# Optimization experiments

Hardware: AMD Instinct MI355X
Metric: run time of the kernel (lower is better)

Reference implementation:

```python
import jax, jax.numpy as jnp
import numpy as np

N_HEAD = 16


def setup_inputs() -> dict:
    key = jax.random.key(0)
    ks = jax.random.split(key, 12)
    B, T, S, D = 64, 1, 448, 1024
    x = jax.random.normal(ks[0], (B, T, D), dtype=jnp.float32)
    k_cache = jax.random.normal(ks[1], (B, S, D), dtype=jnp.float32)
    v_cache = jax.random.normal(ks[2], (B, S, D), dtype=jnp.float32)
    current_index = jax.random.randint(ks[3], (1,), 0, S, dtype=jnp.int64)
    attention_mask = jnp.zeros((1, S), dtype=jnp.float32)
    s = 0.02
    Wq = jax.random.normal(ks[4], (D, D), dtype=jnp.float32) * s
    bq = jax.random.normal(ks[5], (D,), dtype=jnp.float32) * s
    Wk = jax.random.normal(ks[6], (D, D), dtype=jnp.float32) * s  # whisper key proj has no bias
    Wv = jax.random.normal(ks[7], (D, D), dtype=jnp.float32) * s
    bv = jax.random.normal(ks[8], (D,), dtype=jnp.float32) * s
    Wo = jax.random.normal(ks[9], (D, D), dtype=jnp.float32) * s
    bo = jax.random.normal(ks[10], (D,), dtype=jnp.float32) * s
    return {"x": x, "k_cache": k_cache, "v_cache": v_cache,
            "current_index": current_index, "attention_mask": attention_mask,
            "Wq": Wq, "bq": bq, "Wk": Wk, "Wv": Wv, "bv": bv, "Wo": Wo, "bo": bo}


def reference(x, k_cache, v_cache, current_index, attention_mask,
              Wq, bq, Wk, Wv, bv, Wo, bo):
    B, T, D = x.shape            # T == 1 (single decode token)
    S = k_cache.shape[1]         # cache length (448)
    H = N_HEAD
    Dh = D // H
    scale = float(Dh) ** -0.25

    # q/k/v projections of the new token
    q = x @ Wq + bq              # [B, T, D]
    k = x @ Wk                   # [B, T, D]
    v = x @ Wv + bv              # [B, T, D]

    # scatter the new token into the caches at current_index (functional clone+write)
    idx = current_index[0]
    k_upd = jax.lax.dynamic_update_slice(k_cache, k, (0, idx, 0))  # [B, S, D]
    v_upd = jax.lax.dynamic_update_slice(v_cache, v, (0, idx, 0))

    # whisper qkv_attention: scale q and k each by Dh**-0.25
    qh = q.reshape(B, T, H, Dh).transpose(0, 2, 1, 3) * scale      # [B, H, T, Dh]
    kh = k_upd.reshape(B, S, H, Dh).transpose(0, 2, 3, 1) * scale  # [B, H, Dh, S]
    vh = v_upd.reshape(B, S, H, Dh).transpose(0, 2, 1, 3)          # [B, H, S, Dh]

    qk = qh @ kh + attention_mask          # [B, H, T, S]  (mask broadcasts)
    w = jax.nn.softmax(qk, axis=-1)
    wv = (w @ vh).transpose(0, 2, 1, 3).reshape(B, T, D)

    out = wv @ Wo + bo
    return out, k_upd, v_upd
```

## Files before the change

### kernel.cpp

```cpp
#include <hip/hip_runtime.h>

#define B_SZ    64
#define S_LEN   448
#define D_MODEL 1024
#define N_HEAD  16
#define D_HEAD  64
#define CHUNK   28
#define NCH     16

typedef float f4 __attribute__((ext_vector_type(4)));

__global__ __launch_bounds__(256) void gemm_part(
    const float* __restrict__ X,
    const float* __restrict__ W0, const float* __restrict__ W1,
    const float* __restrict__ W2,
    float* __restrict__ P)
{
    const int nt  = blockIdx.x;
    const int kt  = blockIdx.y;
    const int mat = blockIdx.z;
    const float* __restrict__ W = (mat == 0) ? W0 : ((mat == 1) ? W1 : W2);

    const int t  = threadIdx.x;
    const int n  = nt * 64 + (t & 63);
    const int b0 = __builtin_amdgcn_readfirstlane((t >> 6) * 16);
    const int k0 = kt * 128;

    float acc[16];
#pragma unroll
    for (int j = 0; j < 16; ++j) acc[j] = 0.f;

#pragma unroll 8
    for (int k = k0; k < k0 + 128; ++k) {
        const float w = W[k * D_MODEL + n];
#pragma unroll
        for (int j = 0; j < 16; ++j)
            acc[j] += X[(b0 + j) * D_MODEL + k] * w;
    }

    float* p = P + (size_t)(mat * 8 + kt) * (B_SZ * D_MODEL);
#pragma unroll
    for (int j = 0; j < 16; ++j)
        p[(b0 + j) * D_MODEL + n] = acc[j];
}

__global__ __launch_bounds__(256) void reduce_qkv(
    const float* __restrict__ P, float* __restrict__ out)
{
    const int i   = blockIdx.x * 256 + threadIdx.x;
    const int mat = i >> 16;
    const int r   = i & 65535;
    float s = 0.f;
#pragma unroll
    for (int kt = 0; kt < 8; ++kt)
        s += P[(size_t)(mat * 8 + kt) * 65536 + r];
    out[i] = s;
}

__global__ __launch_bounds__(256) void reduce_out(
    const float* __restrict__ P, const float* __restrict__ bo,
    float* __restrict__ out)
{
    const int i = blockIdx.x * 256 + threadIdx.x;
    float s = bo[i & (D_MODEL - 1)];
#pragma unroll
    for (int kt = 0; kt < 8; ++kt)
        s += P[(size_t)kt * 65536 + i];
    out[i] = s;
}

__global__ __launch_bounds__(256) void stream_attn(
    const float* __restrict__ kcache, const float* __restrict__ vcache,
    const float* __restrict__ qws, const float* __restrict__ kws,
    const float* __restrict__ vws,
    const float* __restrict__ bq, const float* __restrict__ bv,
    const float* __restrict__ amask, const int* __restrict__ idxp,
    float* __restrict__ kout, float* __restrict__ vout,
    float* __restrict__ accws, float* __restrict__ mlws)
{
    const int c   = blockIdx.x;
    const int b   = blockIdx.y;
    const int t   = threadIdx.x;
    const int col = t * 4;
    const int h   = t >> 4;
    const int l16 = t & 15;
    const int idx = idxp[0];
    const int s0  = c * CHUNK;

    f4 q = *(const f4*)(qws + b * D_MODEL + col);
    q += *(const f4*)(bq + col);
    const f4 bv4 = *(const f4*)(bv + col);

    float m = -1e30f, l = 0.f;
    f4 acc = (f4)0.f;

#pragma unroll 4
    for (int s = 0; s < CHUNK; ++s) {
        const int srow = s0 + s;
        const bool isn = (srow == idx);
        const size_t roff = (size_t)(b * S_LEN + srow) * D_MODEL + col;
        const float* kp = isn ? (kws + b * D_MODEL + col) : (kcache + roff);
        const float* vp = isn ? (vws + b * D_MODEL + col) : (vcache + roff);
        f4 k4 = *(const f4*)kp;
        f4 v4 = *(const f4*)vp;
        if (isn) v4 += bv4;
        __builtin_nontemporal_store(k4, (f4*)(kout + roff));
        __builtin_nontemporal_store(v4, (f4*)(vout + roff));

        float p = q.x * k4.x + q.y * k4.y + q.z * k4.z + q.w * k4.w;
        p += __shfl_xor(p, 1);
        p += __shfl_xor(p, 2);
        p += __shfl_xor(p, 4);
        p += __shfl_xor(p, 8);
        p = p * 0.125f + amask[srow];

        const float mn = fmaxf(m, p);
        const float f  = __expf(m - mn);
        const float w  = __expf(p - mn);
        l = l * f + w;
        acc.x = acc.x * f + w * v4.x;
        acc.y = acc.y * f + w * v4.y;
        acc.z = acc.z * f + w * v4.z;
        acc.w = acc.w * f + w * v4.w;
        m = mn;
    }

    float* ap = accws + ((size_t)(b * N_HEAD + h) * NCH + c) * D_HEAD + l16 * 4;
    *(f4*)ap = acc;
    if (l16 == 0) {
        const int w = (b * N_HEAD + h) * NCH + c;
        mlws[w * 2]     = m;
        mlws[w * 2 + 1] = l;
    }
}

__global__ __launch_bounds__(256) void combine(
    const float* __restrict__ accws, const float* __restrict__ mlws,
    float* __restrict__ wvws)
{
    const int t = threadIdx.x;
    const int w = blockIdx.x * 4 + (t >> 6);
    const int d = t & 63;

    float M = -1e30f;
#pragma unroll
    for (int c = 0; c < NCH; ++c)
        M = fmaxf(M, mlws[(w * NCH + c) * 2]);
    float L = 0.f, O = 0.f;
#pragma unroll
    for (int c = 0; c < NCH; ++c) {
        const float f = __expf(mlws[(w * NCH + c) * 2] - M);
        L += mlws[(w * NCH + c) * 2 + 1] * f;
        O += accws[(w * NCH + c) * D_HEAD + d] * f;
    }
    const int b = w >> 4, h = w & 15;
    wvws[b * D_MODEL + h * D_HEAD + d] = O / L;
}

extern "C" void kernel_launch(void* const* d_in, const int* in_sizes, int n_in,
                              void* d_out, int out_size, void* d_ws, size_t ws_size,
                              hipStream_t stream) {
    const float* x      = (const float*)d_in[0];
    const float* kcache = (const float*)d_in[1];
    const float* vcache = (const float*)d_in[2];
    const int*   idxp   = (const int*)d_in[3];
    const float* amask  = (const float*)d_in[4];
    const float* Wq     = (const float*)d_in[5];
    const float* bq     = (const float*)d_in[6];
    const float* Wk     = (const float*)d_in[7];
    const float* Wv     = (const float*)d_in[8];
    const float* bv     = (const float*)d_in[9];
    const float* Wo     = (const float*)d_in[10];
    const float* bo     = (const float*)d_in[11];

    float* out  = (float*)d_out;
    float* kout = out + 65536;
    float* vout = kout + (size_t)B_SZ * S_LEN * D_MODEL;

    float* ws    = (float*)d_ws;
    float* qws   = ws;
    float* kws   = ws + 65536;
    float* vws   = ws + 131072;
    float* part  = ws + 196608;
    float* accws = ws + 1769472;
    float* mlws  = ws + 2818048;
    float* wvws  = ws + 2850816;

    gemm_part<<<dim3(16, 8, 3), 256, 0, stream>>>(x, Wq, Wk, Wv, part);
    reduce_qkv<<<768, 256, 0, stream>>>(part, qws);

    stream_attn<<<dim3(NCH, B_SZ), 256, 0, stream>>>(
        kcache, vcache, qws, kws, vws, bq, bv, amask, idxp,
        kout, vout, accws, mlws);

    combine<<<256, 256, 0, stream>>>(accws, mlws, wvws);

    gemm_part<<<dim3(16, 8, 1), 256, 0, stream>>>(wvws, Wo, Wo, Wo, part);
    reduce_out<<<256, 256, 0, stream>>>(part, bo, out);
}
```

Measured before the change: 169.7 us.

## Fuse QKV split-K reduction into attention and prefetch KV rows in registers

Removes the separate reduce_qkv kernel. The attention kernel now sums the 8 split-K partials for q directly, and sums the k/v partials only in blocks whose chunk contains the new index. It also adds an explicit 8-deep register prefetch ring for the K and V cache rows with the loop fully unrolled, so more loads are in flight. The cost is higher register pressure, which may lower occupancy, and each block re-reads the q partials redundantly.

```diff
diff --git a/kernel.cpp b/kernel.cpp
--- a/kernel.cpp
+++ b/kernel.cpp
@@ -7,6 +7,7 @@
 #define D_HEAD  64
 #define CHUNK   28
 #define NCH     16
+#define PF      8
 
 typedef float f4 __attribute__((ext_vector_type(4)));
 
@@ -44,19 +45,6 @@
         p[(b0 + j) * D_MODEL + n] = acc[j];
 }
 
-__global__ __launch_bounds__(256) void reduce_qkv(
-    const float* __restrict__ P, float* __restrict__ out)
-{
-    const int i   = blockIdx.x * 256 + threadIdx.x;
-    const int mat = i >> 16;
-    const int r   = i & 65535;
-    float s = 0.f;
-#pragma unroll
-    for (int kt = 0; kt < 8; ++kt)
-        s += P[(size_t)(mat * 8 + kt) * 65536 + r];
-    out[i] = s;
-}
-
 __global__ __launch_bounds__(256) void reduce_out(
     const float* __restrict__ P, const float* __restrict__ bo,
     float* __restrict__ out)
@@ -71,8 +59,7 @@
 
 __global__ __launch_bounds__(256) void stream_attn(
     const float* __restrict__ kcache, const float* __restrict__ vcache,
-    const float* __restrict__ qws, const float* __restrict__ kws,
-    const float* __restrict__ vws,
+    const float* __restrict__ part,
     const float* __restrict__ bq, const float* __restrict__ bv,
     const float* __restrict__ amask, const int* __restrict__ idxp,
     float* __restrict__ kout, float* __restrict__ vout,
@@ -87,23 +74,45 @@
     const int idx = idxp[0];
     const int s0  = c * CHUNK;
 
-    f4 q = *(const f4*)(qws + b * D_MODEL + col);
-    q += *(const f4*)(bq + col);
-    const f4 bv4 = *(const f4*)(bv + col);
+    f4 q = *(const f4*)(bq + col);
+#pragma unroll
+    for (int kt = 0; kt < 8; ++kt)
+        q += *(const f4*)(part + (size_t)kt * 65536 + b * D_MODEL + col);
+
+    f4 knew = (f4)0.f, vnew = (f4)0.f;
+    const bool hasidx = (idx >= s0) && (idx < s0 + CHUNK);
+    if (hasidx) {
+#pragma unroll
+        for (int kt = 0; kt < 8; ++kt) {
+            knew += *(const f4*)(part + (size_t)(8 + kt)  * 65536 + b * D_MODEL + col);
+            vnew += *(const f4*)(part + (size_t)(16 + kt) * 65536 + b * D_MODEL + col);
+        }
+        vnew += *(const f4*)(bv + col);
+    }
+
+    const size_t base = (size_t)(b * S_LEN + s0) * D_MODEL + col;
+
+    f4 kb[PF], vb[PF];
+#pragma unroll
+    for (int r = 0; r < PF; ++r) {
+        kb[r] = *(const f4*)(kcache + base + (size_t)r * D_MODEL);
+        vb[r] = *(const f4*)(vcache + base + (size_t)r * D_MODEL);
+    }
 
     float m = -1e30f, l = 0.f;
     f4 acc = (f4)0.f;
 
-#pragma unroll 4
+#pragma unroll
     for (int s = 0; s < CHUNK; ++s) {
+        f4 k4 = kb[s & (PF - 1)];
+        f4 v4 = vb[s & (PF - 1)];
+        if (s + PF < CHUNK) {
+            kb[s & (PF - 1)] = *(const f4*)(kcache + base + (size_t)(s + PF) * D_MODEL);
+            vb[s & (PF - 1)] = *(const f4*)(vcache + base + (size_t)(s + PF) * D_MODEL);
+        }
         const int srow = s0 + s;
-        const bool isn = (srow == idx);
-        const size_t roff = (size_t)(b * S_LEN + srow) * D_MODEL + col;
-        const float* kp = isn ? (kws + b * D_MODEL + col) : (kcache + roff);
-        const float* vp = isn ? (vws + b * D_MODEL + col) : (vcache + roff);
-        f4 k4 = *(const f4*)kp;
-        f4 v4 = *(const f4*)vp;
-        if (isn) v4 += bv4;
+        if (srow == idx) { k4 = knew; v4 = vnew; }
+        const size_t roff = base + (size_t)s * D_MODEL;
         __builtin_nontemporal_store(k4, (f4*)(kout + roff));
         __builtin_nontemporal_store(v4, (f4*)(vout + roff));
 
@@ -178,19 +187,15 @@
     float* vout = kout + (size_t)B_SZ * S_LEN * D_MODEL;
 
     float* ws    = (float*)d_ws;
-    float* qws   = ws;
-    float* kws   = ws + 65536;
-    float* vws   = ws + 131072;
-    float* part  = ws + 196608;
-    float* accws = ws + 1769472;
-    float* mlws  = ws + 2818048;
-    float* wvws  = ws + 2850816;
+    float* part  = ws;
+    float* accws = ws + 1572864;
+    float* mlws  = ws + 2621440;
+    float* wvws  = ws + 2654208;
 
     gemm_part<<<dim3(16, 8, 3), 256, 0, stream>>>(x, Wq, Wk, Wv, part);
-    reduce_qkv<<<768, 256, 0, stream>>>(part, qws);
 
     stream_attn<<<dim3(NCH, B_SZ), 256, 0, stream>>>(
-        kcache, vcache, qws, kws, vws, bq, bv, amask, idxp,
+        kcache, vcache, part, bq, bv, amask, idxp,
         kout, vout, accws, mlws);
 
     combine<<<256, 256, 0, stream>>>(accws, mlws, wvws);
```

After: 160.2 us. 5.6% less time.
